# Performance work log

Measured on AMD Instinct MI355X. Metric: run time of the kernel, lower is better.

The kernel has to match this reference:

```python
import jax, jax.numpy as jnp
import numpy as np
from functools import partial


def _lstm_layer(x, W_ih, b_ih, W_hh, b_hh):
    # x: [B, T, D]; W_ih: [4H, D]; W_hh: [4H, H]
    B = x.shape[0]
    H = W_hh.shape[1]
    # Batch the input projection over all timesteps (one big GEMM).
    xg = jnp.einsum('btd,gd->btg', x, W_ih) + b_ih + b_hh  # [B, T, 4H]
    h0 = jnp.zeros((B, H), dtype=x.dtype)
    c0 = jnp.zeros((B, H), dtype=x.dtype)

    def step(carry, xg_t):
        h, c = carry
        gates = xg_t + h @ W_hh.T  # [B, 4H]
        i, f, g, o = jnp.split(gates, 4, axis=-1)
        i = jax.nn.sigmoid(i)
        f = jax.nn.sigmoid(f)
        g = jnp.tanh(g)
        o = jax.nn.sigmoid(o)
        c = f * c + i * g
        h = o * jnp.tanh(c)
        return (h, c), h

    (h_T, c_T), ys = jax.lax.scan(step, (h0, c0), jnp.swapaxes(xg, 0, 1))
    return jnp.swapaxes(ys, 0, 1), h_T, c_T  # [B, T, H], [B, H], [B, H]


def setup_inputs() -> dict:
    key = jax.random.key(0)
    ks = jax.random.split(key, 8)
    B, T, D, H = 64, 512, 1024, 1024
    s = 1.0 / np.sqrt(H)
    return {
        'X': jax.random.normal(ks[0], (B, T, D), jnp.float32),
        'W_ih_0': jax.random.normal(ks[1], (4 * H, D), jnp.float32) * s,
        'b_ih_0': jnp.zeros((4 * H,), jnp.float32),
        'W_hh_0': jax.random.normal(ks[2], (4 * H, H), jnp.float32) * s,
        'b_hh_0': jnp.zeros((4 * H,), jnp.float32),
        'W_ih_1': jax.random.normal(ks[3], (4 * H, H), jnp.float32) * s,
        'b_ih_1': jnp.zeros((4 * H,), jnp.float32),
        'W_hh_1': jax.random.normal(ks[4], (4 * H, H), jnp.float32) * s,
        'b_hh_1': jnp.zeros((4 * H,), jnp.float32),
    }


def reference(X, W_ih_0, b_ih_0, W_hh_0, b_hh_0, W_ih_1, b_ih_1, W_hh_1, b_hh_1):
    out0, h0, c0 = _lstm_layer(X, W_ih_0, b_ih_0, W_hh_0, b_hh_0)
    out1, h1, c1 = _lstm_layer(out0, W_ih_1, b_ih_1, W_hh_1, b_hh_1)
    h_n = jnp.stack([h0, h1], axis=0)  # [num_layers, B, H]
    c_n = jnp.stack([c0, c1], axis=0)
    return out1, (h_n, c_n)
```

## Files before the change

### kernel.cpp

```cpp
#include <hip/hip_runtime.h>
#include <type_traits>

typedef _Float16 half8 __attribute__((ext_vector_type(8)));
typedef _Float16 half4v __attribute__((ext_vector_type(4)));
typedef float f32x4 __attribute__((ext_vector_type(4)));
typedef unsigned long long u64;

struct U128 { u64 a, b; };

#define B_ 64
#define T_ 512
#define H_ 1024
#define G_ 4096
#define K_ 1024
#define MPROJ (B_ * T_)

__global__ void k_f32_to_f16(const float* __restrict__ s, _Float16* __restrict__ d, int n4) {
  int i = blockIdx.x * 256 + threadIdx.x;
  if (i < n4) {
    float4 v = ((const float4*)s)[i];
    half4v o;
    o[0] = (_Float16)v.x; o[1] = (_Float16)v.y; o[2] = (_Float16)v.z; o[3] = (_Float16)v.w;
    ((half4v*)d)[i] = o;
  }
}

__global__ void k_bias(const float* __restrict__ bi0, const float* __restrict__ bh0,
                       const float* __restrict__ bi1, const float* __restrict__ bh1,
                       float* __restrict__ o0, float* __restrict__ o1) {
  int i = blockIdx.x * 256 + threadIdx.x;
  if (i < G_) { o0[i] = bi0[i] + bh0[i]; o1[i] = bi1[i] + bh1[i]; }
}

__global__ void k_zero(uint4* __restrict__ p, int n) {
  int i = blockIdx.x * 256 + threadIdx.x;
  if (i < n) p[i] = make_uint4(0u, 0u, 0u, 0u);
}

template <typename AT>
__global__ __launch_bounds__(256, 2) void k_proj(const AT* __restrict__ A,
                                                 const _Float16* __restrict__ Bw,
                                                 const float* __restrict__ bias,
                                                 _Float16* __restrict__ C) {
  const int NBN = G_ / 128;
  int bm = blockIdx.x / NBN;
  int bn = blockIdx.x % NBN;
  __shared__ __align__(16) _Float16 As[128 * 40];
  __shared__ __align__(16) _Float16 Bs[128 * 40];
  int tid = threadIdx.x;
  int lane = tid & 63, wave = tid >> 6;
  int wm = (wave >> 1) * 64, wn = (wave & 1) * 64;
  int quad = lane >> 4, l16 = lane & 15;
  f32x4 acc[4][4] = {};
  int r = tid >> 1;
  int hc = (tid & 1) * 16;
  const AT* aRow = A + (size_t)(bm * 128 + r) * K_ + hc;
  const _Float16* bRow = Bw + (size_t)(bn * 128 + r) * K_ + hc;
  _Float16* aDst = As + r * 40 + hc;
  _Float16* bDst = Bs + r * 40 + hc;

  for (int kt = 0; kt < K_ / 32; ++kt) {
    if constexpr (std::is_same<AT, float>::value) {
      float tmp[16];
      *(float4*)(tmp + 0)  = *(const float4*)(aRow + 0);
      *(float4*)(tmp + 4)  = *(const float4*)(aRow + 4);
      *(float4*)(tmp + 8)  = *(const float4*)(aRow + 8);
      *(float4*)(tmp + 12) = *(const float4*)(aRow + 12);
      half8 h0, h1;
#pragma unroll
      for (int e = 0; e < 8; ++e) { h0[e] = (_Float16)tmp[e]; h1[e] = (_Float16)tmp[e + 8]; }
      *(half8*)(aDst) = h0;
      *(half8*)(aDst + 8) = h1;
    } else {
      *(half8*)(aDst) = *(const half8*)(aRow);
      *(half8*)(aDst + 8) = *(const half8*)(aRow + 8);
    }
    *(half8*)(bDst) = *(const half8*)(bRow);
    *(half8*)(bDst + 8) = *(const half8*)(bRow + 8);
    __syncthreads();
    half8 af[4], bf[4];
#pragma unroll
    for (int i = 0; i < 4; ++i) af[i] = *(const half8*)(As + (wm + i * 16 + l16) * 40 + quad * 8);
#pragma unroll
    for (int j = 0; j < 4; ++j) bf[j] = *(const half8*)(Bs + (wn + j * 16 + l16) * 40 + quad * 8);
#pragma unroll
    for (int i = 0; i < 4; ++i)
#pragma unroll
      for (int j = 0; j < 4; ++j)
        acc[i][j] = __builtin_amdgcn_mfma_f32_16x16x32_f16(af[i], bf[j], acc[i][j], 0, 0, 0);
    __syncthreads();
    aRow += 32;
    bRow += 32;
  }
#pragma unroll
  for (int j = 0; j < 4; ++j) {
    int n = bn * 128 + wn + j * 16 + l16;
    float bv = bias[n];
#pragma unroll
    for (int i = 0; i < 4; ++i) {
      size_t m0 = (size_t)(bm * 128 + wm + i * 16 + quad * 4);
#pragma unroll
      for (int rr = 0; rr < 4; ++rr)
        C[(m0 + rr) * G_ + n] = (_Float16)(acc[i][j][rr] + bv);
    }
  }
}

__global__ __launch_bounds__(512) void k_fused(
    const _Float16* __restrict__ xg,
    const _Float16* __restrict__ Whh0,
    const _Float16* __restrict__ Wih1,
    const _Float16* __restrict__ Whh1,
    const float* __restrict__ b1,
    _Float16* __restrict__ h0a, _Float16* __restrict__ h0b,
    _Float16* __restrict__ h1a, _Float16* __restrict__ h1b,
    unsigned int* flags,
    float* __restrict__ out32,
    float* __restrict__ hn0, float* __restrict__ cn0,
    float* __restrict__ hn1, float* __restrict__ cn1) {
  int g = blockIdx.x & 3;
  int wid = blockIdx.x >> 2;
  int u0 = wid * 16;
  int b0 = g * 16;
  int tid = threadIdx.x;
  int lane = tid & 63, w = tid >> 6;
  int quad = lane >> 4, l16 = lane & 15;
  unsigned int* gf = flags + (g << 7);

  __shared__ float part[8][8][16][18];
  __shared__ float red[8][16][18];
  __shared__ float cs[2][16][16];
  __shared__ __align__(16) _Float16 wi1_lds[2 * 16 * 1032];
  __shared__ int step_flag;
  ((float*)cs)[tid] = 0.f;
  if (tid == 0) step_flag = 0;

  for (int idx = tid; idx < 2 * 16 * (K_ / 8); idx += 512) {
    int gt2 = idx >> 11;
    int r = (idx >> 7) & 15;
    int c = idx & 127;
    half8 v = *(const half8*)(Wih1 + (size_t)((2 + gt2) * H_ + u0 + r) * K_ + c * 8);
    *(half8*)(wi1_lds + (gt2 * 16 + r) * 1032 + c * 8) = v;
  }

  int ks = w * 128;
  half8 wf0[4][4], wh1[4][4], wi1r[2][4];
#pragma unroll
  for (int gt = 0; gt < 4; ++gt)
#pragma unroll
    for (int kk = 0; kk < 4; ++kk) {
      wf0[gt][kk] = *(const half8*)(Whh0 + (size_t)(gt * H_ + u0 + l16) * K_ + ks + kk * 32 + quad * 8);
      wh1[gt][kk] = *(const half8*)(Whh1 + (size_t)(gt * H_ + u0 + l16) * K_ + ks + kk * 32 + quad * 8);
    }
#pragma unroll
  for (int gt = 0; gt < 2; ++gt)
#pragma unroll
    for (int kk = 0; kk < 4; ++kk)
      wi1r[gt][kk] = *(const half8*)(Wih1 + (size_t)(gt * H_ + u0 + l16) * K_ + ks + kk * 32 + quad * 8);

  int fm = (w & 3) * 4 + quad;
  float b1v[4] = {};
  if (w >= 4) {
#pragma unroll
    for (int gt = 0; gt < 4; ++gt) b1v[gt] = b1[gt * H_ + u0 + l16];
  }
  __syncthreads();

  for (int i = 0; i <= T_; ++i) {
    const _Float16* h0r = (i & 1) ? h0b : h0a;
    _Float16* h0w = (i & 1) ? h0a : h0b;
    const _Float16* h1r = (i & 1) ? h1b : h1a;
    _Float16* h1w = (i & 1) ? h1a : h1b;

    float pxi = 0.f, pxf = 0.f, pxg = 0.f, pxo = 0.f;
    if (w < 4 && i < T_) {
      const _Float16* xr = xg + ((size_t)(b0 + fm) * T_ + i) * G_ + u0 + l16;
      pxi = (float)xr[0];
      pxf = (float)xr[H_];
      pxg = (float)xr[2 * H_];
      pxo = (float)xr[3 * H_];
    }

    half8 af0[4], af1[4];
#pragma unroll
    for (int kk = 0; kk < 4; ++kk) {
      const _Float16* hs = h0r + (size_t)(b0 + l16) * H_ + ks + kk * 32 + quad * 8;
      u64 qlo = __hip_atomic_load((const u64*)hs, __ATOMIC_RELAXED, __HIP_MEMORY_SCOPE_AGENT);
      u64 qhi = __hip_atomic_load(((const u64*)hs) + 1, __ATOMIC_RELAXED, __HIP_MEMORY_SCOPE_AGENT);
      U128 u; u.a = qlo; u.b = qhi;
      af0[kk] = __builtin_bit_cast(half8, u);
    }
#pragma unroll
    for (int kk = 0; kk < 4; ++kk) {
      const _Float16* hs = h1r + (size_t)(b0 + l16) * H_ + ks + kk * 32 + quad * 8;
      u64 qlo = __hip_atomic_load((const u64*)hs, __ATOMIC_RELAXED, __HIP_MEMORY_SCOPE_AGENT);
      u64 qhi = __hip_atomic_load(((const u64*)hs) + 1, __ATOMIC_RELAXED, __HIP_MEMORY_SCOPE_AGENT);
      U128 u; u.a = qlo; u.b = qhi;
      af1[kk] = __builtin_bit_cast(half8, u);
    }

    {
      f32x4 acc[4] = {};
#pragma unroll
      for (int kk = 0; kk < 4; ++kk)
#pragma unroll
        for (int gt = 0; gt < 4; ++gt)
          acc[gt] = __builtin_amdgcn_mfma_f32_16x16x32_f16(af0[kk], wf0[gt][kk], acc[gt], 0, 0, 0);
#pragma unroll
      for (int gt = 0; gt < 4; ++gt)
#pragma unroll
        for (int rr = 0; rr < 4; ++rr)
          part[w][gt][quad * 4 + rr][l16] = acc[gt][rr];
    }
    {
      f32x4 bcc[4] = {};
#pragma unroll
      for (int kk = 0; kk < 4; ++kk) {
        bcc[0] = __builtin_amdgcn_mfma_f32_16x16x32_f16(af0[kk], wi1r[0][kk], bcc[0], 0, 0, 0);
        bcc[1] = __builtin_amdgcn_mfma_f32_16x16x32_f16(af0[kk], wi1r[1][kk], bcc[1], 0, 0, 0);
        half8 w2 = *(const half8*)(wi1_lds + (0 * 16 + l16) * 1032 + ks + kk * 32 + quad * 8);
        bcc[2] = __builtin_amdgcn_mfma_f32_16x16x32_f16(af0[kk], w2, bcc[2], 0, 0, 0);
        half8 w3 = *(const half8*)(wi1_lds + (1 * 16 + l16) * 1032 + ks + kk * 32 + quad * 8);
        bcc[3] = __builtin_amdgcn_mfma_f32_16x16x32_f16(af0[kk], w3, bcc[3], 0, 0, 0);
      }
#pragma unroll
      for (int kk = 0; kk < 4; ++kk)
#pragma unroll
        for (int gt = 0; gt < 4; ++gt)
          bcc[gt] = __builtin_amdgcn_mfma_f32_16x16x32_f16(af1[kk], wh1[gt][kk], bcc[gt], 0, 0, 0);
#pragma unroll
      for (int gt = 0; gt < 4; ++gt)
#pragma unroll
        for (int rr = 0; rr < 4; ++rr)
          part[w][4 + gt][quad * 4 + rr][l16] = bcc[gt][rr];
    }
    __syncthreads();

    {
#pragma unroll
      for (int rr = 0; rr < 4; ++rr) {
        int m = quad * 4 + rr;
        float sum = part[0][w][m][l16];
#pragma unroll
        for (int w2 = 1; w2 < 8; ++w2) sum += part[w2][w][m][l16];
        red[w][m][l16] = sum;
      }
    }
    __syncthreads();

    float ph = 0.f;
    size_t poidx = 0;
    if (w < 4) {
      if (i < T_) {
        int m = fm, n = l16;
        float iv = red[0][m][n] + pxi;
        float fv = red[1][m][n] + pxf;
        float gv = red[2][m][n] + pxg;
        float ov = red[3][m][n] + pxo;
        float si = 1.f / (1.f + __expf(-iv));
        float sf = 1.f / (1.f + __expf(-fv));
        float so = 1.f / (1.f + __expf(-ov));
        float ag = fabsf(gv), eg = __expf(-2.f * ag);
        float tg = (1.f - eg) / (1.f + eg);
        tg = (gv < 0.f) ? -tg : tg;
        float c = sf * cs[0][m][n] + si * tg;
        cs[0][m][n] = c;
        float ac = fabsf(c), ec = __expf(-2.f * ac);
        float th = (1.f - ec) / (1.f + ec);
        th = (c < 0.f) ? -th : th;
        float h = so * th;
        unsigned short hu = __builtin_bit_cast(unsigned short, (_Float16)h);
        unsigned other = __shfl_xor((unsigned)hu, 1, 64);
        if ((l16 & 1) == 0) {
          unsigned packed = (unsigned)hu | (other << 16);
          __hip_atomic_store((unsigned*)(h0w + (size_t)(b0 + m) * H_ + u0 + l16), packed,
                             __ATOMIC_RELAXED, __HIP_MEMORY_SCOPE_AGENT);
        }
        if (i == T_ - 1) {
          hn0[(size_t)(b0 + m) * H_ + u0 + n] = h;
          cn0[(size_t)(b0 + m) * H_ + u0 + n] = c;
        }
      }
    } else {
      if (i >= 1) {
        int m = fm, n = l16;
        int j = i - 1;
        float iv = red[4][m][n] + b1v[0];
        float fv = red[5][m][n] + b1v[1];
        float gv = red[6][m][n] + b1v[2];
        float ov = red[7][m][n] + b1v[3];
        float si = 1.f / (1.f + __expf(-iv));
        float sf = 1.f / (1.f + __expf(-fv));
        float so = 1.f / (1.f + __expf(-ov));
        float ag = fabsf(gv), eg = __expf(-2.f * ag);
        float tg = (1.f - eg) / (1.f + eg);
        tg = (gv < 0.f) ? -tg : tg;
        float c = sf * cs[1][m][n] + si * tg;
        cs[1][m][n] = c;
        float ac = fabsf(c), ec = __expf(-2.f * ac);
        float th = (1.f - ec) / (1.f + ec);
        th = (c < 0.f) ? -th : th;
        float h = so * th;
        unsigned short hu = __builtin_bit_cast(unsigned short, (_Float16)h);
        unsigned other = __shfl_xor((unsigned)hu, 1, 64);
        if ((l16 & 1) == 0) {
          unsigned packed = (unsigned)hu | (other << 16);
          __hip_atomic_store((unsigned*)(h1w + (size_t)(b0 + m) * H_ + u0 + l16), packed,
                             __ATOMIC_RELAXED, __HIP_MEMORY_SCOPE_AGENT);
        }
        ph = h;
        poidx = ((size_t)(b0 + m) * T_ + j) * H_ + u0 + n;
        if (j == T_ - 1) {
          hn1[(size_t)(b0 + m) * H_ + u0 + n] = h;
          cn1[(size_t)(b0 + m) * H_ + u0 + n] = c;
        }
      }
    }
    __syncthreads();

    if (i == T_) {
      if (w >= 4) out32[poidx] = ph;
      break;
    }
    if (w == 1 && lane == 0)
      __hip_atomic_store(gf + wid, (unsigned)(i + 1),
                         __ATOMIC_RELAXED, __HIP_MEMORY_SCOPE_AGENT);
    if (w >= 4 && i >= 1) out32[poidx] = ph;

    unsigned tgt = (unsigned)(i + 1);
    if (w == 0) {
      for (;;) {
        unsigned v = __hip_atomic_load(gf + lane, __ATOMIC_RELAXED, __HIP_MEMORY_SCOPE_AGENT);
        if (__all(v >= tgt)) break;
        __builtin_amdgcn_s_sleep(1);
      }
      asm volatile("" ::: "memory");
      if (lane == 0) __atomic_store_n(&step_flag, (int)tgt, __ATOMIC_RELEASE);
    } else {
      while (__atomic_load_n(&step_flag, __ATOMIC_ACQUIRE) < (int)tgt)
        __builtin_amdgcn_s_sleep(1);
      asm volatile("" ::: "memory");
    }
  }
}

extern "C" void kernel_launch(void* const* d_in, const int* in_sizes, int n_in,
                              void* d_out, int out_size, void* d_ws, size_t ws_size,
                              hipStream_t stream) {
  (void)in_sizes; (void)n_in; (void)out_size;
  const float* X    = (const float*)d_in[0];
  const float* Wih0 = (const float*)d_in[1];
  const float* bih0 = (const float*)d_in[2];
  const float* Whh0 = (const float*)d_in[3];
  const float* bhh0 = (const float*)d_in[4];
  const float* Wih1 = (const float*)d_in[5];
  const float* bih1 = (const float*)d_in[6];
  const float* Whh1 = (const float*)d_in[7];
  const float* bhh1 = (const float*)d_in[8];
  float* out = (float*)d_out;
  char* ws = (char*)d_ws;

  constexpr size_t SZW = (size_t)G_ * K_ * 2;
  constexpr size_t OFF_B0   = 4 * SZW;
  constexpr size_t OFF_B1   = OFF_B0 + 16384;
  constexpr size_t OFF_CNT  = OFF_B1 + 16384;
  constexpr size_t OFF_HBUF = OFF_CNT + 16384;
  constexpr size_t OFF_XG   = OFF_HBUF + 4 * 131072;
  constexpr size_t NEED     = OFF_XG + (size_t)MPROJ * G_ * 2;
  if (ws_size < NEED) return;

  _Float16* Wih0h = (_Float16*)(ws + 0 * SZW);
  _Float16* Whh0h = (_Float16*)(ws + 1 * SZW);
  _Float16* Wih1h = (_Float16*)(ws + 2 * SZW);
  _Float16* Whh1h = (_Float16*)(ws + 3 * SZW);
  float* b0s = (float*)(ws + OFF_B0);
  float* b1s = (float*)(ws + OFF_B1);
  unsigned int* flgs = (unsigned int*)(ws + OFF_CNT);
  _Float16* hb = (_Float16*)(ws + OFF_HBUF);
  _Float16* h0a = hb;
  _Float16* h0b = hb + 65536;
  _Float16* h1a = hb + 131072;
  _Float16* h1b = hb + 196608;
  _Float16* xgp = (_Float16*)(ws + OFF_XG);

  k_f32_to_f16<<<4096, 256, 0, stream>>>(Wih0, Wih0h, G_ * K_ / 4);
  k_f32_to_f16<<<4096, 256, 0, stream>>>(Whh0, Whh0h, G_ * K_ / 4);
  k_f32_to_f16<<<4096, 256, 0, stream>>>(Wih1, Wih1h, G_ * K_ / 4);
  k_f32_to_f16<<<4096, 256, 0, stream>>>(Whh1, Whh1h, G_ * K_ / 4);
  k_bias<<<16, 256, 0, stream>>>(bih0, bhh0, bih1, bhh1, b0s, b1s);
  k_zero<<<132, 256, 0, stream>>>((uint4*)(ws + OFF_CNT), (int)((16384 + 4 * 131072) / 16));

  const int projGrid = (MPROJ / 128) * (G_ / 128);
  k_proj<float><<<dim3(projGrid), dim3(256), 0, stream>>>(X, Wih0h, b0s, xgp);

  {
    const _Float16* a0 = xgp;
    const _Float16* a1 = Whh0h;
    const _Float16* a2 = Wih1h;
    const _Float16* a3 = Whh1h;
    const float* a4 = b1s;
    _Float16* a5 = h0a;
    _Float16* a6 = h0b;
    _Float16* a7 = h1a;
    _Float16* a8 = h1b;
    unsigned int* a9 = flgs;
    float* a10 = out;
    float* a11 = out + 33554432;
    float* a12 = out + 33554432 + 131072;
    float* a13 = out + 33554432 + 65536;
    float* a14 = out + 33554432 + 131072 + 65536;
    void* args[15] = {&a0, &a1, &a2, &a3, &a4, &a5, &a6, &a7,
                      &a8, &a9, &a10, &a11, &a12, &a13, &a14};
    hipLaunchCooperativeKernel((void*)k_fused, dim3(256), dim3(512), args, 0, stream);
  }
}
```

Before: 4.954 ms.

## Fuse layer-0 input projection into persistent recurrent kernel, removing separate GEMM

Drops the standalone xg GEMM kernel and its 256 MB fp16 intermediate. Each step, the persistent cooperative kernel now computes the next timestep's layer-0 input projection with MFMAs, using X converted to fp16, Wih0 read from global/L2, and staging through a new shared buffer. It overlaps this work with the flag spin-wait. The cost is that Wih0 tiles are re-read from global every step, and the per-step critical path gains compute if the wait does not hide it.

Result: slower. 7.049 ms (+42.3%).

```diff
diff --git a/kernel.cpp b/kernel.cpp
--- a/kernel.cpp
+++ b/kernel.cpp
@@ -1,5 +1,4 @@
 #include <hip/hip_runtime.h>
-#include <type_traits>
 
 typedef _Float16 half8 __attribute__((ext_vector_type(8)));
 typedef _Float16 half4v __attribute__((ext_vector_type(4)));
@@ -13,7 +12,6 @@
 #define H_ 1024
 #define G_ 4096
 #define K_ 1024
-#define MPROJ (B_ * T_)
 
 __global__ void k_f32_to_f16(const float* __restrict__ s, _Float16* __restrict__ d, int n4) {
   int i = blockIdx.x * 256 + threadIdx.x;
@@ -37,81 +35,14 @@
   if (i < n) p[i] = make_uint4(0u, 0u, 0u, 0u);
 }
 
-template <typename AT>
-__global__ __launch_bounds__(256, 2) void k_proj(const AT* __restrict__ A,
-                                                 const _Float16* __restrict__ Bw,
-                                                 const float* __restrict__ bias,
-                                                 _Float16* __restrict__ C) {
-  const int NBN = G_ / 128;
-  int bm = blockIdx.x / NBN;
-  int bn = blockIdx.x % NBN;
-  __shared__ __align__(16) _Float16 As[128 * 40];
-  __shared__ __align__(16) _Float16 Bs[128 * 40];
-  int tid = threadIdx.x;
-  int lane = tid & 63, wave = tid >> 6;
-  int wm = (wave >> 1) * 64, wn = (wave & 1) * 64;
-  int quad = lane >> 4, l16 = lane & 15;
-  f32x4 acc[4][4] = {};
-  int r = tid >> 1;
-  int hc = (tid & 1) * 16;
-  const AT* aRow = A + (size_t)(bm * 128 + r) * K_ + hc;
-  const _Float16* bRow = Bw + (size_t)(bn * 128 + r) * K_ + hc;
-  _Float16* aDst = As + r * 40 + hc;
-  _Float16* bDst = Bs + r * 40 + hc;
-
-  for (int kt = 0; kt < K_ / 32; ++kt) {
-    if constexpr (std::is_same<AT, float>::value) {
-      float tmp[16];
-      *(float4*)(tmp + 0)  = *(const float4*)(aRow + 0);
-      *(float4*)(tmp + 4)  = *(const float4*)(aRow + 4);
-      *(float4*)(tmp + 8)  = *(const float4*)(aRow + 8);
-      *(float4*)(tmp + 12) = *(const float4*)(aRow + 12);
-      half8 h0, h1;
-#pragma unroll
-      for (int e = 0; e < 8; ++e) { h0[e] = (_Float16)tmp[e]; h1[e] = (_Float16)tmp[e + 8]; }
-      *(half8*)(aDst) = h0;
-      *(half8*)(aDst + 8) = h1;
-    } else {
-      *(half8*)(aDst) = *(const half8*)(aRow);
-      *(half8*)(aDst + 8) = *(const half8*)(aRow + 8);
-    }
-    *(half8*)(bDst) = *(const half8*)(bRow);
-    *(half8*)(bDst + 8) = *(const half8*)(bRow + 8);
-    __syncthreads();
-    half8 af[4], bf[4];
-#pragma unroll
-    for (int i = 0; i < 4; ++i) af[i] = *(const half8*)(As + (wm + i * 16 + l16) * 40 + quad * 8);
-#pragma unroll
-    for (int j = 0; j < 4; ++j) bf[j] = *(const half8*)(Bs + (wn + j * 16 + l16) * 40 + quad * 8);
-#pragma unroll
-    for (int i = 0; i < 4; ++i)
-#pragma unroll
-      for (int j = 0; j < 4; ++j)
-        acc[i][j] = __builtin_amdgcn_mfma_f32_16x16x32_f16(af[i], bf[j], acc[i][j], 0, 0, 0);
-    __syncthreads();
-    aRow += 32;
-    bRow += 32;
-  }
-#pragma unroll
-  for (int j = 0; j < 4; ++j) {
-    int n = bn * 128 + wn + j * 16 + l16;
-    float bv = bias[n];
-#pragma unroll
-    for (int i = 0; i < 4; ++i) {
-      size_t m0 = (size_t)(bm * 128 + wm + i * 16 + quad * 4);
-#pragma unroll
-      for (int rr = 0; rr < 4; ++rr)
-        C[(m0 + rr) * G_ + n] = (_Float16)(acc[i][j][rr] + bv);
-    }
-  }
-}
-
 __global__ __launch_bounds__(512) void k_fused(
-    const _Float16* __restrict__ xg,
+    const _Float16* __restrict__ Xh,
+    const _Float16* __restrict__ Wih0,
     const _Float16* __restrict__ Whh0,
     const _Float16* __restrict__ Wih1,
     const _Float16* __restrict__ Whh1,
-    const float* __restrict__ b1,
+    const float* __restrict__ bias0,
+    const float* __restrict__ bias1,
     _Float16* __restrict__ h0a, _Float16* __restrict__ h0b,
     _Float16* __restrict__ h1a, _Float16* __restrict__ h1b,
     unsigned int* flags,
@@ -121,7 +52,7 @@
   int g = blockIdx.x & 3;
   int wid = blockIdx.x >> 2;
   int u0 = wid * 16;
-  int b0 = g * 16;
+  int bb = g * 16;
   int tid = threadIdx.x;
   int lane = tid & 63, w = tid >> 6;
   int quad = lane >> 4, l16 = lane & 15;
@@ -129,6 +60,7 @@
 
   __shared__ float part[8][8][16][18];
   __shared__ float red[8][16][18];
+  __shared__ float part_x[4][2][16][17];
   __shared__ float cs[2][16][16];
   __shared__ __align__(16) _Float16 wi1_lds[2 * 16 * 1032];
   __shared__ int step_flag;
@@ -159,10 +91,30 @@
       wi1r[gt][kk] = *(const half8*)(Wih1 + (size_t)(gt * H_ + u0 + l16) * K_ + ks + kk * 32 + quad * 8);
 
   int fm = (w & 3) * 4 + quad;
-  float b1v[4] = {};
-  if (w >= 4) {
-#pragma unroll
-    for (int gt = 0; gt < 4; ++gt) b1v[gt] = b1[gt * H_ + u0 + l16];
+  float b0v[4] = {}, b1v[4] = {};
+  if (w < 4) {
+#pragma unroll
+    for (int gt = 0; gt < 4; ++gt) b0v[gt] = bias0[gt * H_ + u0 + l16];
+  } else {
+#pragma unroll
+    for (int gt = 0; gt < 4; ++gt) b1v[gt] = bias1[gt * H_ + u0 + l16];
+  }
+
+  int gx = w & 3, kh = w >> 2;
+  const _Float16* wpB = Wih0 + (size_t)(gx * H_ + u0 + l16) * K_ + kh * 512 + quad * 8;
+  const _Float16* xB0 = Xh + ((size_t)(bb + l16) * T_) * K_ + kh * 512 + quad * 8;
+
+  {
+    const _Float16* xB = xB0;
+    f32x4 xcc = {};
+#pragma unroll
+    for (int kk = 0; kk < 16; ++kk) {
+      half8 wv = *(const half8*)(wpB + kk * 32);
+      half8 xv = *(const half8*)(xB + kk * 32);
+      xcc = __builtin_amdgcn_mfma_f32_16x16x32_f16(xv, wv, xcc, 0, 0, 0);
+    }
+#pragma unroll
+    for (int rr = 0; rr < 4; ++rr) part_x[gx][kh][quad * 4 + rr][l16] = xcc[rr];
   }
   __syncthreads();
 
@@ -172,19 +124,10 @@
     const _Float16* h1r = (i & 1) ? h1b : h1a;
     _Float16* h1w = (i & 1) ? h1a : h1b;
 
-    float pxi = 0.f, pxf = 0.f, pxg = 0.f, pxo = 0.f;
-    if (w < 4 && i < T_) {
-      const _Float16* xr = xg + ((size_t)(b0 + fm) * T_ + i) * G_ + u0 + l16;
-      pxi = (float)xr[0];
-      pxf = (float)xr[H_];
-      pxg = (float)xr[2 * H_];
-      pxo = (float)xr[3 * H_];
-    }
-
     half8 af0[4], af1[4];
 #pragma unroll
     for (int kk = 0; kk < 4; ++kk) {
-      const _Float16* hs = h0r + (size_t)(b0 + l16) * H_ + ks + kk * 32 + quad * 8;
+      const _Float16* hs = h0r + (size_t)(bb + l16) * H_ + ks + kk * 32 + quad * 8;
       u64 qlo = __hip_atomic_load((const u64*)hs, __ATOMIC_RELAXED, __HIP_MEMORY_SCOPE_AGENT);
       u64 qhi = __hip_atomic_load(((const u64*)hs) + 1, __ATOMIC_RELAXED, __HIP_MEMORY_SCOPE_AGENT);
       U128 u; u.a = qlo; u.b = qhi;
@@ -192,7 +135,7 @@
     }
 #pragma unroll
     for (int kk = 0; kk < 4; ++kk) {
-      const _Float16* hs = h1r + (size_t)(b0 + l16) * H_ + ks + kk * 32 + quad * 8;
+      const _Float16* hs = h1r + (size_t)(bb + l16) * H_ + ks + kk * 32 + quad * 8;
       u64 qlo = __hip_atomic_load((const u64*)hs, __ATOMIC_RELAXED, __HIP_MEMORY_SCOPE_AGENT);
       u64 qhi = __hip_atomic_load(((const u64*)hs) + 1, __ATOMIC_RELAXED, __HIP_MEMORY_SCOPE_AGENT);
       U128 u; u.a = qlo; u.b = qhi;
@@ -253,10 +196,10 @@
     if (w < 4) {
       if (i < T_) {
         int m = fm, n = l16;
-        float iv = red[0][m][n] + pxi;
-        float fv = red[1][m][n] + pxf;
-        float gv = red[2][m][n] + pxg;
-        float ov = red[3][m][n] + pxo;
+        float iv = red[0][m][n] + part_x[0][0][m][n] + part_x[0][1][m][n] + b0v[0];
+        float fv = red[1][m][n] + part_x[1][0][m][n] + part_x[1][1][m][n] + b0v[1];
+        float gv = red[2][m][n] + part_x[2][0][m][n] + part_x[2][1][m][n] + b0v[2];
+        float ov = red[3][m][n] + part_x[3][0][m][n] + part_x[3][1][m][n] + b0v[3];
         float si = 1.f / (1.f + __expf(-iv));
         float sf = 1.f / (1.f + __expf(-fv));
         float so = 1.f / (1.f + __expf(-ov));
@@ -273,12 +216,12 @@
         unsigned other = __shfl_xor((unsigned)hu, 1, 64);
         if ((l16 & 1) == 0) {
           unsigned packed = (unsigned)hu | (other << 16);
-          __hip_atomic_store((unsigned*)(h0w + (size_t)(b0 + m) * H_ + u0 + l16), packed,
+          __hip_atomic_store((unsigned*)(h0w + (size_t)(bb + m) * H_ + u0 + l16), packed,
                              __ATOMIC_RELAXED, __HIP_MEMORY_SCOPE_AGENT);
         }
         if (i == T_ - 1) {
-          hn0[(size_t)(b0 + m) * H_ + u0 + n] = h;
-          cn0[(size_t)(b0 + m) * H_ + u0 + n] = c;
+          hn0[(size_t)(bb + m) * H_ + u0 + n] = h;
+          cn0[(size_t)(bb + m) * H_ + u0 + n] = c;
         }
       }
     } else {
@@ -305,14 +248,14 @@
         unsigned other = __shfl_xor((unsigned)hu, 1, 64);
         if ((l16 & 1) == 0) {
           unsigned packed = (unsigned)hu | (other << 16);
-          __hip_atomic_store((unsigned*)(h1w + (size_t)(b0 + m) * H_ + u0 + l16), packed,
+          __hip_atomic_store((unsigned*)(h1w + (size_t)(bb + m) * H_ + u0 + l16), packed,
                              __ATOMIC_RELAXED, __HIP_MEMORY_SCOPE_AGENT);
         }
         ph = h;
-        poidx = ((size_t)(b0 + m) * T_ + j) * H_ + u0 + n;
+        poidx = ((size_t)(bb + m) * T_ + j) * H_ + u0 + n;
         if (j == T_ - 1) {
-          hn1[(size_t)(b0 + m) * H_ + u0 + n] = h;
-          cn1[(size_t)(b0 + m) * H_ + u0 + n] = c;
+          hn1[(size_t)(bb + m) * H_ + u0 + n] = h;
+          cn1[(size_t)(bb + m) * H_ + u0 + n] = c;
         }
       }
     }
@@ -326,6 +269,19 @@
       __hip_atomic_store(gf + wid, (unsigned)(i + 1),
                          __ATOMIC_RELAXED, __HIP_MEMORY_SCOPE_AGENT);
     if (w >= 4 && i >= 1) out32[poidx] = ph;
+
+    if (i + 1 < T_) {
+      const _Float16* xB = xB0 + (size_t)(i + 1) * K_;
+      f32x4 xcc = {};
+#pragma unroll
+      for (int kk = 0; kk < 16; ++kk) {
+        half8 wv = *(const half8*)(wpB + kk * 32);
+        half8 xv = *(const half8*)(xB + kk * 32);
+        xcc = __builtin_amdgcn_mfma_f32_16x16x32_f16(xv, wv, xcc, 0, 0, 0);
+      }
+#pragma unroll
+      for (int rr = 0; rr < 4; ++rr) part_x[gx][kh][quad * 4 + rr][l16] = xcc[rr];
+    }
 
     unsigned tgt = (unsigned)(i + 1);
     if (w == 0) {
@@ -365,8 +321,8 @@
   constexpr size_t OFF_B1   = OFF_B0 + 16384;
   constexpr size_t OFF_CNT  = OFF_B1 + 16384;
   constexpr size_t OFF_HBUF = OFF_CNT + 16384;
-  constexpr size_t OFF_XG   = OFF_HBUF + 4 * 131072;
-  constexpr size_t NEED     = OFF_XG + (size_t)MPROJ * G_ * 2;
+  constexpr size_t OFF_XH   = OFF_HBUF + 4 * 131072;
+  constexpr size_t NEED     = OFF_XH + (size_t)B_ * T_ * K_ * 2;
   if (ws_size < NEED) return;
 
   _Float16* Wih0h = (_Float16*)(ws + 0 * SZW);
@@ -381,36 +337,36 @@
   _Float16* h0b = hb + 65536;
   _Float16* h1a = hb + 131072;
   _Float16* h1b = hb + 196608;
-  _Float16* xgp = (_Float16*)(ws + OFF_XG);
+  _Float16* Xhp = (_Float16*)(ws + OFF_XH);
 
   k_f32_to_f16<<<4096, 256, 0, stream>>>(Wih0, Wih0h, G_ * K_ / 4);
   k_f32_to_f16<<<4096, 256, 0, stream>>>(Whh0, Whh0h, G_ * K_ / 4);
   k_f32_to_f16<<<4096, 256, 0, stream>>>(Wih1, Wih1h, G_ * K_ / 4);
   k_f32_to_f16<<<4096, 256, 0, stream>>>(Whh1, Whh1h, G_ * K_ / 4);
+  k_f32_to_f16<<<32768, 256, 0, stream>>>(X, Xhp, B_ * T_ * K_ / 4);
   k_bias<<<16, 256, 0, stream>>>(bih0, bhh0, bih1, bhh1, b0s, b1s);
   k_zero<<<132, 256, 0, stream>>>((uint4*)(ws + OFF_CNT), (int)((16384 + 4 * 131072) / 16));
 
-  const int projGrid = (MPROJ / 128) * (G_ / 128);
-  k_proj<float><<<dim3(projGrid), dim3(256), 0, stream>>>(X, Wih0h, b0s, xgp);
-
   {
-    const _Float16* a0 = xgp;
-    const _Float16* a1 = Whh0h;
-    const _Float16* a2 = Wih1h;
-    const _Float16* a3 = Whh1h;
-    const float* a4 = b1s;
-    _Float16* a5 = h0a;
-    _Float16* a6 = h0b;
-    _Float16* a7 = h1a;
-    _Float16* a8 = h1b;
-    unsigned int* a9 = flgs;
-    float* a10 = out;
-    float* a11 = out + 33554432;
-    float* a12 = out + 33554432 + 131072;
-    float* a13 = out + 33554432 + 65536;
-    float* a14 = out + 33554432 + 131072 + 65536;
-    void* args[15] = {&a0, &a1, &a2, &a3, &a4, &a5, &a6, &a7,
-                      &a8, &a9, &a10, &a11, &a12, &a13, &a14};
+    const _Float16* a0 = Xhp;
+    const _Float16* a1 = Wih0h;
+    const _Float16* a2 = Whh0h;
+    const _Float16* a3 = Wih1h;
+    const _Float16* a4 = Whh1h;
+    const float* a5 = b0s;
+    const float* a6 = b1s;
+    _Float16* a7 = h0a;
+    _Float16* a8 = h0b;
+    _Float16* a9 = h1a;
+    _Float16* a10 = h1b;
+    unsigned int* a11 = flgs;
+    float* a12 = out;
+    float* a13 = out + 33554432;
+    float* a14 = out + 33554432 + 131072;
+    float* a15 = out + 33554432 + 65536;
+    float* a16 = out + 33554432 + 131072 + 65536;
+    void* args[17] = {&a0, &a1, &a2, &a3, &a4, &a5, &a6, &a7, &a8,
+                      &a9, &a10, &a11, &a12, &a13, &a14, &a15, &a16};
     hipLaunchCooperativeKernel((void*)k_fused, dim3(256), dim3(512), args, 0, stream);
   }
 }
```
